# Kernel optimization log

Hardware: AMD Instinct MI355X
Metric: run time of the kernel (lower is better)

Reference implementation:

```python
import jax, jax.numpy as jnp
import numpy as np

TOP_K = 2
LB_WEIGHT = 0.01
Z_WEIGHT = 0.001


def setup_inputs() -> dict:
    key = jax.random.key(0)
    ks = jax.random.split(key, 5)
    B, S, D, F, E = 4, 2048, 1024, 2048, 8
    x = jax.random.normal(ks[0], (B, S, D), dtype=jnp.float32)
    Wr = jax.random.normal(ks[1], (D, E), dtype=jnp.float32) / np.sqrt(D).astype(np.float32)
    Wg = jax.random.normal(ks[2], (E, D, F), dtype=jnp.float32) / np.sqrt(D).astype(np.float32)
    Wu = jax.random.normal(ks[3], (E, D, F), dtype=jnp.float32) / np.sqrt(D).astype(np.float32)
    Wd = jax.random.normal(ks[4], (E, F, D), dtype=jnp.float32) / np.sqrt(F).astype(np.float32)
    return {"x": x, "Wr": Wr, "Wg": Wg, "Wu": Wu, "Wd": Wd}


def reference(x, Wr, Wg, Wu, Wd):
    B, S, D = x.shape
    E = Wr.shape[1]
    xf = x.reshape(-1, D)                       # [T, D]
    T = xf.shape[0]

    logits = xf @ Wr                            # [T, E]
    probs = jax.nn.softmax(logits, axis=-1)
    topv, topi = jax.lax.top_k(probs, TOP_K)    # [T, K]
    topv = topv / jnp.sum(topv, axis=-1, keepdims=True)

    # combine[t, e] = renormalized top-k prob if expert e selected for token t, else 0
    onehot = jax.nn.one_hot(topi, E, dtype=x.dtype)          # [T, K, E]
    combine = jnp.sum(onehot * topv[..., None], axis=1)      # [T, E]

    out = jnp.zeros_like(xf)
    for e in range(E):  # fixed small expert count; dense compute masked by combine weights
        h = jax.nn.silu(xf @ Wg[e]) * (xf @ Wu[e])           # [T, F] SwiGLU
        out = out + combine[:, e:e + 1] * (h @ Wd[e])

    # auxiliary losses
    counts = jnp.sum(onehot, axis=(0, 1))                    # [E] tokens routed per expert
    f_i = counts / (T * TOP_K)
    P_i = jnp.mean(probs, axis=0)
    load_balance = E * jnp.sum(f_i * P_i)
    z_loss = jnp.mean(jax.nn.logsumexp(logits, axis=-1) ** 2)
    aux_loss = LB_WEIGHT * load_balance + Z_WEIGHT * z_loss

    return out.reshape(B, S, D), aux_loss
```

## Files before the change

### kernel.cpp

```cpp
#include <hip/hip_runtime.h>
#include <cstdint>

#define T_TOK 8192
#define Dm 1024
#define Fm 2048
#define Em 8

typedef unsigned short u16;
typedef __attribute__((ext_vector_type(8))) short short8;
typedef __attribute__((ext_vector_type(4))) float floatx4;

__device__ __forceinline__ u16 f2bf(float f) {
  union { float f; unsigned u; } v; v.f = f;
  unsigned r = v.u + 0x7fffu + ((v.u >> 16) & 1u);
  return (u16)(r >> 16);
}

__device__ __forceinline__ void gld_lds16(const void* g, void* l) {
  __builtin_amdgcn_global_load_lds(
      (const __attribute__((address_space(1))) void*)g,
      (__attribute__((address_space(3))) void*)l, 16, 0, 0);
}

__global__ void zero_meta(int* counts, int* offc, float* psum, float* zsum) {
  int t = threadIdx.x;
  if (t < 8) { counts[t] = 0; offc[t] = 0; psum[t] = 0.f; }
  if (t == 8) zsum[0] = 0.f;
}

__global__ __launch_bounds__(256) void prep_kernel(
    const float* __restrict__ Wg, const float* __restrict__ Wu, const float* __restrict__ Wd,
    u16* __restrict__ WgT, u16* __restrict__ WuT, u16* __restrict__ WdT,
    const float* __restrict__ x, const float* __restrict__ Wr, u16* __restrict__ xb,
    int* __restrict__ topi, float* __restrict__ topw,
    int* __restrict__ counts, float* __restrict__ psum, float* __restrict__ zsum) {
  __shared__ __align__(16) char smem[33056];
  int tid = threadIdx.x;
  if (blockIdx.x >= 256) {
    u16* tile = (u16*)smem;
    int bid = blockIdx.x - 256;
    int m = bid >> 9, t = bid & 511;
    int type = m >> 3, e = m & 7;
    const float* src; u16* dst; int R, C, csh;
    if (type == 0)      { src = Wg; dst = WgT; R = Dm; C = Fm; csh = 5; }
    else if (type == 1) { src = Wu; dst = WuT; R = Dm; C = Fm; csh = 5; }
    else                { src = Wd; dst = WdT; R = Fm; C = Dm; csh = 4; }
    int ty = t >> csh, tx = t & ((1 << csh) - 1);
    int r0 = ty * 64, c0 = tx * 64;
    const float* s = src + (size_t)e * R * C;
    u16* d = dst + (size_t)e * C * R;
#pragma unroll
    for (int p = 0; p < 16; ++p) {
      int idx = p * 256 + tid;
      int i = idx >> 6, j = idx & 63;
      tile[i * 66 + j] = f2bf(s[(size_t)(r0 + i) * C + (c0 + j)]);
    }
    __syncthreads();
#pragma unroll
    for (int p = 0; p < 16; ++p) {
      int idx = p * 256 + tid;
      int i = idx >> 6, j = idx & 63;
      d[(size_t)(c0 + i) * R + (r0 + j)] = tile[j * 66 + i];
    }
    return;
  }
  int rb = blockIdx.x;
  float* wr_s = (float*)smem;
  float (*redf)[9] = (float(*)[9])(smem + 32768);
  int (*redi)[8] = (int(*)[8])(smem + 32768 + 144);
  for (int i = tid; i < Dm * Em; i += 256) wr_s[i] = Wr[i];
  __syncthreads();
  int wv = tid >> 6, lane = tid & 63;
  float pl[8] = {0, 0, 0, 0, 0, 0, 0, 0};
  float zl = 0.f;
  int cl[8] = {0, 0, 0, 0, 0, 0, 0, 0};
  for (int it = 0; it < 8; ++it) {
    int t = (rb * 4 + wv) * 8 + it;
    const float* xt = x + (size_t)t * Dm;
    u16* xbt = xb + (size_t)t * Dm;
    float acc[8] = {0, 0, 0, 0, 0, 0, 0, 0};
#pragma unroll
    for (int i = 0; i < 16; ++i) {
      int dd = i * 64 + lane;
      float xv = xt[dd];
      xbt[dd] = f2bf(xv);
#pragma unroll
      for (int e2 = 0; e2 < 8; ++e2) acc[e2] += xv * wr_s[dd * 8 + e2];
    }
#pragma unroll
    for (int e2 = 0; e2 < 8; ++e2) {
      float v = acc[e2];
      for (int o = 32; o > 0; o >>= 1) v += __shfl_down(v, o);
      acc[e2] = v;
    }
    if (lane == 0) {
      float m = acc[0];
#pragma unroll
      for (int e2 = 1; e2 < 8; ++e2) m = fmaxf(m, acc[e2]);
      float p[8]; float s = 0.f;
#pragma unroll
      for (int e2 = 0; e2 < 8; ++e2) { p[e2] = expf(acc[e2] - m); s += p[e2]; }
      float inv = 1.f / s;
#pragma unroll
      for (int e2 = 0; e2 < 8; ++e2) { p[e2] *= inv; pl[e2] += p[e2]; }
      float lse = m + logf(s);
      zl += lse * lse;
      int i1 = 0;
#pragma unroll
      for (int e2 = 1; e2 < 8; ++e2) if (p[e2] > p[i1]) i1 = e2;
      int i2 = -1; float b2 = -1e30f;
#pragma unroll
      for (int e2 = 0; e2 < 8; ++e2)
        if (e2 != i1 && p[e2] > b2) { b2 = p[e2]; i2 = e2; }
      float ssum = p[i1] + p[i2];
      topi[2 * t] = i1; topi[2 * t + 1] = i2;
      topw[2 * t] = p[i1] / ssum; topw[2 * t + 1] = p[i2] / ssum;
      cl[i1]++; cl[i2]++;
    }
  }
  if (lane == 0) {
#pragma unroll
    for (int e2 = 0; e2 < 8; ++e2) { redf[wv][e2] = pl[e2]; redi[wv][e2] = cl[e2]; }
    redf[wv][8] = zl;
  }
  __syncthreads();
  if (tid < 8) {
    atomicAdd(&psum[tid], redf[0][tid] + redf[1][tid] + redf[2][tid] + redf[3][tid]);
    atomicAdd(&counts[tid], redi[0][tid] + redi[1][tid] + redi[2][tid] + redi[3][tid]);
  } else if (tid == 8) {
    atomicAdd(zsum, redf[0][8] + redf[1][8] + redf[2][8] + redf[3][8]);
  }
}

__global__ __launch_bounds__(256) void scatter_kernel(
    const int* __restrict__ topi, const float* __restrict__ topw,
    const int* __restrict__ counts, const float* __restrict__ psum, const float* __restrict__ zsum,
    int* __restrict__ offc, int* __restrict__ etok, float* __restrict__ ew,
    int* __restrict__ slots, int* __restrict__ bases, float* __restrict__ out_aux) {
  __shared__ int lcnt[8];
  __shared__ int lbase[8];
  __shared__ int basesS[8];
  int tid = threadIdx.x;
  if (blockIdx.x == 0 && tid == 0) {
    float lb = 0.f;
    for (int e = 0; e < 8; ++e)
      lb += ((float)counts[e] / (2.f * T_TOK)) * (psum[e] / (float)T_TOK);
    lb *= 8.f;
    float z = zsum[0] / (float)T_TOK;
    *out_aux = 0.01f * lb + 0.001f * z;
  }
  if (tid < 8) {
    lcnt[tid] = 0;
    int b = 0;
    for (int e = 0; e < tid; ++e) b += counts[e];
    basesS[tid] = b;
    if (blockIdx.x == 0) bases[tid] = b;
  }
  __syncthreads();
  int t = blockIdx.x * 256 + tid;
  int e0 = topi[2 * t], e1 = topi[2 * t + 1];
  int lp0 = atomicAdd(&lcnt[e0], 1);
  int lp1 = atomicAdd(&lcnt[e1], 1);
  __syncthreads();
  if (tid < 8) lbase[tid] = atomicAdd(&offc[tid], lcnt[tid]);
  __syncthreads();
  int p0 = basesS[e0] + lbase[e0] + lp0;
  etok[p0] = t; ew[p0] = topw[2 * t]; slots[2 * t] = p0;
  int p1 = basesS[e1] + lbase[e1] + lp1;
  etok[p1] = t; ew[p1] = topw[2 * t + 1]; slots[2 * t + 1] = p1;
}

__global__ __launch_bounds__(256, 3) void gemm1_kernel(
    const u16* __restrict__ xb, const u16* __restrict__ WgT, const u16* __restrict__ WuT,
    u16* __restrict__ h, const int* __restrict__ etok,
    const int* __restrict__ counts, const int* __restrict__ bases) {
  const int e = blockIdx.z;
  const int Ne = counts[e];
  const int m0 = blockIdx.y * 128;
  if (m0 >= Ne) return;
  const int n0 = blockIdx.x * 64;
  const int be = bases[e];

  __shared__ __align__(16) u16 As[128 * 64];
  __shared__ __align__(16) u16 Bgs[64 * 64];
  __shared__ __align__(16) u16 Bus[64 * 64];

  const int tid = threadIdx.x;
  const int wv = tid >> 6, lane = tid & 63;
  const int wr = wv >> 1, wc = wv & 1;
  const int srow = tid >> 3;
  const int cg = (tid & 7) ^ (srow & 7);
  const u16* wg_e = WgT + (size_t)e * Fm * Dm;
  const u16* wu_e = WuT + (size_t)e * Fm * Dm;

  const u16* ag[4]; const u16* bgp[2]; const u16* bup[2];
#pragma unroll
  for (int j = 0; j < 4; ++j) {
    int row = 32 * j + srow;
    int rr = m0 + row; rr = rr < Ne ? rr : Ne - 1;
    int tok = etok[be + rr];
    ag[j] = xb + (size_t)tok * Dm + cg * 8;
  }
#pragma unroll
  for (int j = 0; j < 2; ++j) {
    int row = 32 * j + srow;
    bgp[j] = wg_e + (size_t)(n0 + row) * Dm + cg * 8;
    bup[j] = wu_e + (size_t)(n0 + row) * Dm + cg * 8;
  }
  const int lbase = 8 * wv * 64 + lane * 8;

  floatx4 accg[4][2], accu[4][2];
#pragma unroll
  for (int mi = 0; mi < 4; ++mi)
#pragma unroll
    for (int ni = 0; ni < 2; ++ni) { accg[mi][ni] = (floatx4)0.f; accu[mi][ni] = (floatx4)0.f; }

  for (int k0 = 0; k0 < Dm; k0 += 64) {
    __syncthreads();
#pragma unroll
    for (int j = 0; j < 4; ++j) gld_lds16(ag[j] + k0, &As[lbase + 32 * j * 64]);
#pragma unroll
    for (int j = 0; j < 2; ++j) {
      int lo = lbase + 32 * j * 64;
      gld_lds16(bgp[j] + k0, &Bgs[lo]);
      gld_lds16(bup[j] + k0, &Bus[lo]);
    }
    __syncthreads();
#pragma unroll
    for (int ks = 0; ks < 2; ++ks) {
      short8 af[4], bgf[2], buf_[2];
      const int col = lane & 15, quad = lane >> 4;
      const int c = ks * 4 + quad;
#pragma unroll
      for (int mi = 0; mi < 4; ++mi) {
        int row = wr * 64 + mi * 16 + col;
        af[mi] = *(const short8*)&As[row * 64 + ((c ^ (row & 7)) << 3)];
      }
#pragma unroll
      for (int ni = 0; ni < 2; ++ni) {
        int row = wc * 32 + ni * 16 + col;
        int o = row * 64 + ((c ^ (row & 7)) << 3);
        bgf[ni] = *(const short8*)&Bgs[o];
        buf_[ni] = *(const short8*)&Bus[o];
      }
#pragma unroll
      for (int mi = 0; mi < 4; ++mi)
#pragma unroll
        for (int ni = 0; ni < 2; ++ni) {
          accg[mi][ni] = __builtin_amdgcn_mfma_f32_16x16x32_bf16(af[mi], bgf[ni], accg[mi][ni], 0, 0, 0);
          accu[mi][ni] = __builtin_amdgcn_mfma_f32_16x16x32_bf16(af[mi], buf_[ni], accu[mi][ni], 0, 0, 0);
        }
    }
  }
  const int col = lane & 15, quad = lane >> 4;
#pragma unroll
  for (int mi = 0; mi < 4; ++mi)
#pragma unroll
    for (int ni = 0; ni < 2; ++ni) {
      int f = n0 + wc * 32 + ni * 16 + col;
#pragma unroll
      for (int r = 0; r < 4; ++r) {
        int lrow = wr * 64 + mi * 16 + quad * 4 + r;
        if (m0 + lrow < Ne) {
          float gv = accg[mi][ni][r];
          float hv = (gv / (1.f + expf(-gv))) * accu[mi][ni][r];
          h[(size_t)(be + m0 + lrow) * Fm + f] = f2bf(hv);
        }
      }
    }
}

__global__ __launch_bounds__(256, 3) void gemm2_kernel(
    const u16* __restrict__ h, const u16* __restrict__ WdT, float* __restrict__ h2,
    const float* __restrict__ ew,
    const int* __restrict__ counts, const int* __restrict__ bases) {
  const int e = blockIdx.z;
  const int Ne = counts[e];
  const int m0 = blockIdx.y * 128;
  if (m0 >= Ne) return;
  const int n0 = blockIdx.x * 64;
  const int be = bases[e];

  __shared__ __align__(16) u16 As[128 * 64];
  __shared__ __align__(16) u16 Bs[64 * 64];
  __shared__ float wS[128];

  const int tid = threadIdx.x;
  if (tid < 128) {
    int rr = m0 + tid; rr = rr < Ne ? rr : Ne - 1;
    wS[tid] = ew[be + rr];
  }
  const int wv = tid >> 6, lane = tid & 63;
  const int wr = wv >> 1, wc = wv & 1;
  const int srow = tid >> 3;
  const int cg = (tid & 7) ^ (srow & 7);
  const u16* wd_e = WdT + (size_t)e * Dm * Fm;

  const u16* ap[4]; const u16* bp[2];
#pragma unroll
  for (int j = 0; j < 4; ++j) {
    int row = 32 * j + srow;
    int rr = m0 + row; rr = rr < Ne ? rr : Ne - 1;
    ap[j] = h + (size_t)(be + rr) * Fm + cg * 8;
  }
#pragma unroll
  for (int j = 0; j < 2; ++j) {
    int row = 32 * j + srow;
    bp[j] = wd_e + (size_t)(n0 + row) * Fm + cg * 8;
  }
  const int lbase = 8 * wv * 64 + lane * 8;

  floatx4 acc[4][2];
#pragma unroll
  for (int mi = 0; mi < 4; ++mi)
#pragma unroll
    for (int ni = 0; ni < 2; ++ni) acc[mi][ni] = (floatx4)0.f;

  for (int k0 = 0; k0 < Fm; k0 += 64) {
    __syncthreads();
#pragma unroll
    for (int j = 0; j < 4; ++j) gld_lds16(ap[j] + k0, &As[lbase + 32 * j * 64]);
#pragma unroll
    for (int j = 0; j < 2; ++j) gld_lds16(bp[j] + k0, &Bs[lbase + 32 * j * 64]);
    __syncthreads();
#pragma unroll
    for (int ks = 0; ks < 2; ++ks) {
      short8 af[4], bf[2];
      const int col = lane & 15, quad = lane >> 4;
      const int c = ks * 4 + quad;
#pragma unroll
      for (int mi = 0; mi < 4; ++mi) {
        int row = wr * 64 + mi * 16 + col;
        af[mi] = *(const short8*)&As[row * 64 + ((c ^ (row & 7)) << 3)];
      }
#pragma unroll
      for (int ni = 0; ni < 2; ++ni) {
        int row = wc * 32 + ni * 16 + col;
        bf[ni] = *(const short8*)&Bs[row * 64 + ((c ^ (row & 7)) << 3)];
      }
#pragma unroll
      for (int mi = 0; mi < 4; ++mi)
#pragma unroll
        for (int ni = 0; ni < 2; ++ni)
          acc[mi][ni] = __builtin_amdgcn_mfma_f32_16x16x32_bf16(af[mi], bf[ni], acc[mi][ni], 0, 0, 0);
    }
  }
  const int col = lane & 15, quad = lane >> 4;
#pragma unroll
  for (int mi = 0; mi < 4; ++mi)
#pragma unroll
    for (int ni = 0; ni < 2; ++ni) {
      int oc = n0 + wc * 32 + ni * 16 + col;
#pragma unroll
      for (int r = 0; r < 4; ++r) {
        int lrow = wr * 64 + mi * 16 + quad * 4 + r;
        if (m0 + lrow < Ne)
          h2[(size_t)(be + m0 + lrow) * Dm + oc] = acc[mi][ni][r] * wS[lrow];
      }
    }
}

__global__ __launch_bounds__(256) void combine_kernel(
    const float* __restrict__ h2, const int* __restrict__ slots, float* __restrict__ out) {
  int t = blockIdx.x;
  int d4 = threadIdx.x;
  int s0 = slots[2 * t], s1 = slots[2 * t + 1];
  const float4* r0 = (const float4*)(h2 + (size_t)s0 * Dm);
  const float4* r1 = (const float4*)(h2 + (size_t)s1 * Dm);
  float4 a = r0[d4], b = r1[d4];
  float4 o = make_float4(a.x + b.x, a.y + b.y, a.z + b.z, a.w + b.w);
  ((float4*)(out + (size_t)t * Dm))[d4] = o;
}

extern "C" void kernel_launch(void* const* d_in, const int* in_sizes, int n_in,
                              void* d_out, int out_size, void* d_ws, size_t ws_size,
                              hipStream_t stream) {
  const float* x = (const float*)d_in[0];
  const float* Wr = (const float*)d_in[1];
  const float* Wg = (const float*)d_in[2];
  const float* Wu = (const float*)d_in[3];
  const float* Wd = (const float*)d_in[4];
  float* out = (float*)d_out;

  char* p = (char*)d_ws;
  auto take = [&](size_t bytes) { char* r = p; p += (bytes + 255) & ~(size_t)255; return r; };
  u16* WgT = (u16*)take((size_t)Em * Fm * Dm * 2);
  u16* WuT = (u16*)take((size_t)Em * Fm * Dm * 2);
  u16* WdT = (u16*)take((size_t)Em * Dm * Fm * 2);
  u16* xb = (u16*)take((size_t)T_TOK * Dm * 2);
  u16* gh = (u16*)take((size_t)2 * T_TOK * Fm * 2);
  int* topi = (int*)take((size_t)T_TOK * 2 * 4);
  float* topw = (float*)take((size_t)T_TOK * 2 * 4);
  int* etok = (int*)take((size_t)2 * T_TOK * 4);
  float* ew = (float*)take((size_t)2 * T_TOK * 4);
  int* slots = (int*)take((size_t)2 * T_TOK * 4);
  int* counts = (int*)take(64);
  int* bases = (int*)take(64);
  int* offc = (int*)take(64);
  float* psum = (float*)take(64);
  float* zsum = (float*)take(64);
  float* h2 = (float*)WgT;

  zero_meta<<<1, 64, 0, stream>>>(counts, offc, psum, zsum);
  prep_kernel<<<dim3(24 * 512 + 256), 256, 0, stream>>>(
      Wg, Wu, Wd, WgT, WuT, WdT, x, Wr, xb, topi, topw, counts, psum, zsum);
  scatter_kernel<<<dim3(T_TOK / 256), 256, 0, stream>>>(
      topi, topw, counts, psum, zsum, offc, etok, ew, slots, bases, out + (size_t)T_TOK * Dm);
  gemm1_kernel<<<dim3(Fm / 64, 64, Em), 256, 0, stream>>>(xb, WgT, WuT, gh, etok, counts, bases);
  gemm2_kernel<<<dim3(Dm / 64, 64, Em), 256, 0, stream>>>(gh, WdT, h2, ew, counts, bases);
  combine_kernel<<<dim3(T_TOK), 256, 0, stream>>>(h2, slots, out);
}
```

Baseline: 523.5 us.

## Enlarge MoE GEMM tiles and add 4-stage async LDS pipeline with priority hints

Both expert GEMMs move to 512-thread blocks with larger output tiles (256x128 for gate/up, 256x256 for down) and a K-step of 32 staged through a 4-deep ring of LDS buffers. Global-to-LDS loads are issued three stages ahead, and each step has one barrier gated by explicit vmcnt waits. MFMA bursts are wrapped in s_setprio so that memory traffic overlaps compute and fewer barriers are paid per unit of work. In exchange, register and LDS use per block rise (128KB LDS), partially filled M tiles waste more work, and the grids have fewer blocks.

```diff
diff --git a/kernel.cpp b/kernel.cpp
--- a/kernel.cpp
+++ b/kernel.cpp
@@ -170,97 +170,122 @@
   etok[p1] = t; ew[p1] = topw[2 * t + 1]; slots[2 * t + 1] = p1;
 }
 
-__global__ __launch_bounds__(256, 3) void gemm1_kernel(
+__global__ __launch_bounds__(512, 2) void gemm1_kernel(
     const u16* __restrict__ xb, const u16* __restrict__ WgT, const u16* __restrict__ WuT,
     u16* __restrict__ h, const int* __restrict__ etok,
     const int* __restrict__ counts, const int* __restrict__ bases) {
   const int e = blockIdx.z;
   const int Ne = counts[e];
-  const int m0 = blockIdx.y * 128;
+  const int m0 = blockIdx.y * 256;
   if (m0 >= Ne) return;
-  const int n0 = blockIdx.x * 64;
+  const int n0 = blockIdx.x * 128;
   const int be = bases[e];
 
-  __shared__ __align__(16) u16 As[128 * 64];
-  __shared__ __align__(16) u16 Bgs[64 * 64];
-  __shared__ __align__(16) u16 Bus[64 * 64];
+  __shared__ __align__(16) u16 lds[4 * 16384];
 
   const int tid = threadIdx.x;
-  const int wv = tid >> 6, lane = tid & 63;
-  const int wr = wv >> 1, wc = wv & 1;
-  const int srow = tid >> 3;
-  const int cg = (tid & 7) ^ (srow & 7);
+  const int lane = tid & 63, wv = tid >> 6;
+  const int wm = wv >> 2, wn = wv & 3;
+  const int col = lane & 15, quad = lane >> 4;
+
+  const int srow = tid >> 2;
+  const int cg = (tid & 3) ^ ((srow >> 2) & 3);
+  const int ldst = tid * 8;
+
   const u16* wg_e = WgT + (size_t)e * Fm * Dm;
   const u16* wu_e = WuT + (size_t)e * Fm * Dm;
 
-  const u16* ag[4]; const u16* bgp[2]; const u16* bup[2];
-#pragma unroll
-  for (int j = 0; j < 4; ++j) {
-    int row = 32 * j + srow;
-    int rr = m0 + row; rr = rr < Ne ? rr : Ne - 1;
-    int tok = etok[be + rr];
-    ag[j] = xb + (size_t)tok * Dm + cg * 8;
-  }
+  const u16* ag[2];
 #pragma unroll
   for (int j = 0; j < 2; ++j) {
-    int row = 32 * j + srow;
-    bgp[j] = wg_e + (size_t)(n0 + row) * Dm + cg * 8;
-    bup[j] = wu_e + (size_t)(n0 + row) * Dm + cg * 8;
-  }
-  const int lbase = 8 * wv * 64 + lane * 8;
-
-  floatx4 accg[4][2], accu[4][2];
-#pragma unroll
-  for (int mi = 0; mi < 4; ++mi)
+    int row = m0 + j * 128 + srow;
+    int rr = row < Ne ? row : Ne - 1;
+    ag[j] = xb + (size_t)etok[be + rr] * Dm + cg * 8;
+  }
+  const u16* bgp = wg_e + (size_t)(n0 + srow) * Dm + cg * 8;
+  const u16* bup = wu_e + (size_t)(n0 + srow) * Dm + cg * 8;
+
+  floatx4 accg[8][2], accu[8][2];
+#pragma unroll
+  for (int mi = 0; mi < 8; ++mi)
 #pragma unroll
     for (int ni = 0; ni < 2; ++ni) { accg[mi][ni] = (floatx4)0.f; accu[mi][ni] = (floatx4)0.f; }
 
-  for (int k0 = 0; k0 < Dm; k0 += 64) {
-    __syncthreads();
-#pragma unroll
-    for (int j = 0; j < 4; ++j) gld_lds16(ag[j] + k0, &As[lbase + 32 * j * 64]);
-#pragma unroll
-    for (int j = 0; j < 2; ++j) {
-      int lo = lbase + 32 * j * 64;
-      gld_lds16(bgp[j] + k0, &Bgs[lo]);
-      gld_lds16(bup[j] + k0, &Bus[lo]);
-    }
-    __syncthreads();
-#pragma unroll
-    for (int ks = 0; ks < 2; ++ks) {
-      short8 af[4], bgf[2], buf_[2];
-      const int col = lane & 15, quad = lane >> 4;
-      const int c = ks * 4 + quad;
-#pragma unroll
-      for (int mi = 0; mi < 4; ++mi) {
-        int row = wr * 64 + mi * 16 + col;
-        af[mi] = *(const short8*)&As[row * 64 + ((c ^ (row & 7)) << 3)];
+#define G1_STAGE_A(t) { u16* b_ = &lds[((t) & 3) * 16384]; int k0_ = (t) * 32; \
+    gld_lds16(ag[0] + k0_, b_ + ldst); gld_lds16(ag[1] + k0_, b_ + 4096 + ldst); }
+#define G1_STAGE_B(t) { u16* b_ = &lds[((t) & 3) * 16384]; int k0_ = (t) * 32; \
+    gld_lds16(bgp + k0_, b_ + 8192 + ldst); gld_lds16(bup + k0_, b_ + 12288 + ldst); }
+
+  G1_STAGE_A(0); G1_STAGE_B(0);
+  G1_STAGE_A(1); G1_STAGE_B(1);
+  G1_STAGE_A(2); G1_STAGE_B(2);
+  asm volatile("s_waitcnt vmcnt(8)" ::: "memory");
+  __builtin_amdgcn_s_barrier();
+  asm volatile("" ::: "memory");
+  __builtin_amdgcn_sched_barrier(0);
+
+  for (int t = 0; t < 32; ++t) {
+    const u16* Ab = &lds[(t & 3) * 16384];
+    const u16* Gb = Ab + 8192;
+    const u16* Ub = Ab + 12288;
+    short8 bgf[2], buf_[2], af[4];
+#pragma unroll
+    for (int ni = 0; ni < 2; ++ni) {
+      int row = wn * 32 + ni * 16 + col;
+      int o = row * 32 + (((quad ^ (row >> 2)) & 3) << 3);
+      bgf[ni] = *(const short8*)&Gb[o];
+      buf_[ni] = *(const short8*)&Ub[o];
+    }
+#pragma unroll
+    for (int mi = 0; mi < 4; ++mi) {
+      int row = wm * 128 + mi * 16 + col;
+      af[mi] = *(const short8*)&Ab[row * 32 + (((quad ^ (row >> 2)) & 3) << 3)];
+    }
+    if (t + 3 < 32) G1_STAGE_A(t + 3);
+    __builtin_amdgcn_s_setprio(1);
+#pragma unroll
+    for (int mi = 0; mi < 4; ++mi)
+#pragma unroll
+      for (int ni = 0; ni < 2; ++ni) {
+        accg[mi][ni] = __builtin_amdgcn_mfma_f32_16x16x32_bf16(af[mi], bgf[ni], accg[mi][ni], 0, 0, 0);
+        accu[mi][ni] = __builtin_amdgcn_mfma_f32_16x16x32_bf16(af[mi], buf_[ni], accu[mi][ni], 0, 0, 0);
       }
+    __builtin_amdgcn_s_setprio(0);
+#pragma unroll
+    for (int mi = 0; mi < 4; ++mi) {
+      int row = wm * 128 + (mi + 4) * 16 + col;
+      af[mi] = *(const short8*)&Ab[row * 32 + (((quad ^ (row >> 2)) & 3) << 3)];
+    }
+    if (t + 3 < 32) G1_STAGE_B(t + 3);
+    __builtin_amdgcn_s_setprio(1);
+#pragma unroll
+    for (int mi = 0; mi < 4; ++mi)
 #pragma unroll
       for (int ni = 0; ni < 2; ++ni) {
-        int row = wc * 32 + ni * 16 + col;
-        int o = row * 64 + ((c ^ (row & 7)) << 3);
-        bgf[ni] = *(const short8*)&Bgs[o];
-        buf_[ni] = *(const short8*)&Bus[o];
+        accg[mi + 4][ni] = __builtin_amdgcn_mfma_f32_16x16x32_bf16(af[mi], bgf[ni], accg[mi + 4][ni], 0, 0, 0);
+        accu[mi + 4][ni] = __builtin_amdgcn_mfma_f32_16x16x32_bf16(af[mi], buf_[ni], accu[mi + 4][ni], 0, 0, 0);
       }
-#pragma unroll
-      for (int mi = 0; mi < 4; ++mi)
-#pragma unroll
-        for (int ni = 0; ni < 2; ++ni) {
-          accg[mi][ni] = __builtin_amdgcn_mfma_f32_16x16x32_bf16(af[mi], bgf[ni], accg[mi][ni], 0, 0, 0);
-          accu[mi][ni] = __builtin_amdgcn_mfma_f32_16x16x32_bf16(af[mi], buf_[ni], accu[mi][ni], 0, 0, 0);
-        }
-    }
-  }
-  const int col = lane & 15, quad = lane >> 4;
-#pragma unroll
-  for (int mi = 0; mi < 4; ++mi)
+    __builtin_amdgcn_s_setprio(0);
+    if (t + 3 < 32)      { asm volatile("s_waitcnt vmcnt(8)" ::: "memory"); }
+    else if (t + 2 < 32) { asm volatile("s_waitcnt vmcnt(4)" ::: "memory"); }
+    else if (t + 1 < 32) { asm volatile("s_waitcnt vmcnt(0)" ::: "memory"); }
+    if (t + 1 < 32) {
+      __builtin_amdgcn_s_barrier();
+      asm volatile("" ::: "memory");
+      __builtin_amdgcn_sched_barrier(0);
+    }
+  }
+#undef G1_STAGE_A
+#undef G1_STAGE_B
+
+#pragma unroll
+  for (int mi = 0; mi < 8; ++mi)
 #pragma unroll
     for (int ni = 0; ni < 2; ++ni) {
-      int f = n0 + wc * 32 + ni * 16 + col;
+      int f = n0 + wn * 32 + ni * 16 + col;
 #pragma unroll
       for (int r = 0; r < 4; ++r) {
-        int lrow = wr * 64 + mi * 16 + quad * 4 + r;
+        int lrow = wm * 128 + mi * 16 + quad * 4 + r;
         if (m0 + lrow < Ne) {
           float gv = accg[mi][ni][r];
           float hv = (gv / (1.f + expf(-gv))) * accu[mi][ni][r];
@@ -270,90 +295,118 @@
     }
 }
 
-__global__ __launch_bounds__(256, 3) void gemm2_kernel(
+__global__ __launch_bounds__(512, 2) void gemm2_kernel(
     const u16* __restrict__ h, const u16* __restrict__ WdT, float* __restrict__ h2,
     const float* __restrict__ ew,
     const int* __restrict__ counts, const int* __restrict__ bases) {
   const int e = blockIdx.z;
   const int Ne = counts[e];
-  const int m0 = blockIdx.y * 128;
+  const int m0 = blockIdx.y * 256;
   if (m0 >= Ne) return;
-  const int n0 = blockIdx.x * 64;
+  const int n0 = blockIdx.x * 256;
   const int be = bases[e];
 
-  __shared__ __align__(16) u16 As[128 * 64];
-  __shared__ __align__(16) u16 Bs[64 * 64];
-  __shared__ float wS[128];
+  __shared__ __align__(16) u16 lds[4 * 16384];
+  __shared__ float wS[256];
 
   const int tid = threadIdx.x;
-  if (tid < 128) {
+  if (tid < 256) {
     int rr = m0 + tid; rr = rr < Ne ? rr : Ne - 1;
     wS[tid] = ew[be + rr];
   }
-  const int wv = tid >> 6, lane = tid & 63;
-  const int wr = wv >> 1, wc = wv & 1;
-  const int srow = tid >> 3;
-  const int cg = (tid & 7) ^ (srow & 7);
+  const int lane = tid & 63, wv = tid >> 6;
+  const int wm = wv >> 2, wn = wv & 3;
+  const int col = lane & 15, quad = lane >> 4;
+
+  const int srow = tid >> 2;
+  const int cg = (tid & 3) ^ ((srow >> 2) & 3);
+  const int ldst = tid * 8;
+
   const u16* wd_e = WdT + (size_t)e * Dm * Fm;
 
-  const u16* ap[4]; const u16* bp[2];
-#pragma unroll
-  for (int j = 0; j < 4; ++j) {
-    int row = 32 * j + srow;
-    int rr = m0 + row; rr = rr < Ne ? rr : Ne - 1;
+  const u16* ap[2]; const u16* bp[2];
+#pragma unroll
+  for (int j = 0; j < 2; ++j) {
+    int row = m0 + j * 128 + srow;
+    int rr = row < Ne ? row : Ne - 1;
     ap[j] = h + (size_t)(be + rr) * Fm + cg * 8;
-  }
-#pragma unroll
-  for (int j = 0; j < 2; ++j) {
-    int row = 32 * j + srow;
-    bp[j] = wd_e + (size_t)(n0 + row) * Fm + cg * 8;
-  }
-  const int lbase = 8 * wv * 64 + lane * 8;
-
-  floatx4 acc[4][2];
-#pragma unroll
-  for (int mi = 0; mi < 4; ++mi)
-#pragma unroll
-    for (int ni = 0; ni < 2; ++ni) acc[mi][ni] = (floatx4)0.f;
-
-  for (int k0 = 0; k0 < Fm; k0 += 64) {
-    __syncthreads();
-#pragma unroll
-    for (int j = 0; j < 4; ++j) gld_lds16(ap[j] + k0, &As[lbase + 32 * j * 64]);
-#pragma unroll
-    for (int j = 0; j < 2; ++j) gld_lds16(bp[j] + k0, &Bs[lbase + 32 * j * 64]);
-    __syncthreads();
-#pragma unroll
-    for (int ks = 0; ks < 2; ++ks) {
-      short8 af[4], bf[2];
-      const int col = lane & 15, quad = lane >> 4;
-      const int c = ks * 4 + quad;
-#pragma unroll
-      for (int mi = 0; mi < 4; ++mi) {
-        int row = wr * 64 + mi * 16 + col;
-        af[mi] = *(const short8*)&As[row * 64 + ((c ^ (row & 7)) << 3)];
-      }
-#pragma unroll
-      for (int ni = 0; ni < 2; ++ni) {
-        int row = wc * 32 + ni * 16 + col;
-        bf[ni] = *(const short8*)&Bs[row * 64 + ((c ^ (row & 7)) << 3)];
-      }
-#pragma unroll
-      for (int mi = 0; mi < 4; ++mi)
-#pragma unroll
-        for (int ni = 0; ni < 2; ++ni)
-          acc[mi][ni] = __builtin_amdgcn_mfma_f32_16x16x32_bf16(af[mi], bf[ni], acc[mi][ni], 0, 0, 0);
-    }
-  }
-  const int col = lane & 15, quad = lane >> 4;
-#pragma unroll
-  for (int mi = 0; mi < 4; ++mi)
-#pragma unroll
-    for (int ni = 0; ni < 2; ++ni) {
-      int oc = n0 + wc * 32 + ni * 16 + col;
+    bp[j] = wd_e + (size_t)(n0 + j * 128 + srow) * Fm + cg * 8;
+  }
+
+  floatx4 acc[8][4];
+#pragma unroll
+  for (int mi = 0; mi < 8; ++mi)
+#pragma unroll
+    for (int ni = 0; ni < 4; ++ni) acc[mi][ni] = (floatx4)0.f;
+
+#define G2_STAGE_A(t) { u16* b_ = &lds[((t) & 3) * 16384]; int k0_ = (t) * 32; \
+    gld_lds16(ap[0] + k0_, b_ + ldst); gld_lds16(ap[1] + k0_, b_ + 4096 + ldst); }
+#define G2_STAGE_B(t) { u16* b_ = &lds[((t) & 3) * 16384]; int k0_ = (t) * 32; \
+    gld_lds16(bp[0] + k0_, b_ + 8192 + ldst); gld_lds16(bp[1] + k0_, b_ + 12288 + ldst); }
+
+  G2_STAGE_A(0); G2_STAGE_B(0);
+  G2_STAGE_A(1); G2_STAGE_B(1);
+  G2_STAGE_A(2); G2_STAGE_B(2);
+  asm volatile("s_waitcnt vmcnt(8)" ::: "memory");
+  __builtin_amdgcn_s_barrier();
+  asm volatile("" ::: "memory");
+  __builtin_amdgcn_sched_barrier(0);
+
+  for (int t = 0; t < 64; ++t) {
+    const u16* Ab = &lds[(t & 3) * 16384];
+    const u16* Bb = Ab + 8192;
+    short8 bf[4], af[4];
+#pragma unroll
+    for (int ni = 0; ni < 4; ++ni) {
+      int row = wn * 64 + ni * 16 + col;
+      bf[ni] = *(const short8*)&Bb[row * 32 + (((quad ^ (row >> 2)) & 3) << 3)];
+    }
+#pragma unroll
+    for (int mi = 0; mi < 4; ++mi) {
+      int row = wm * 128 + mi * 16 + col;
+      af[mi] = *(const short8*)&Ab[row * 32 + (((quad ^ (row >> 2)) & 3) << 3)];
+    }
+    if (t + 3 < 64) G2_STAGE_A(t + 3);
+    __builtin_amdgcn_s_setprio(1);
+#pragma unroll
+    for (int mi = 0; mi < 4; ++mi)
+#pragma unroll
+      for (int ni = 0; ni < 4; ++ni)
+        acc[mi][ni] = __builtin_amdgcn_mfma_f32_16x16x32_bf16(af[mi], bf[ni], acc[mi][ni], 0, 0, 0);
+    __builtin_amdgcn_s_setprio(0);
+#pragma unroll
+    for (int mi = 0; mi < 4; ++mi) {
+      int row = wm * 128 + (mi + 4) * 16 + col;
+      af[mi] = *(const short8*)&Ab[row * 32 + (((quad ^ (row >> 2)) & 3) << 3)];
+    }
+    if (t + 3 < 64) G2_STAGE_B(t + 3);
+    __builtin_amdgcn_s_setprio(1);
+#pragma unroll
+    for (int mi = 0; mi < 4; ++mi)
+#pragma unroll
+      for (int ni = 0; ni < 4; ++ni)
+        acc[mi + 4][ni] = __builtin_amdgcn_mfma_f32_16x16x32_bf16(af[mi], bf[ni], acc[mi + 4][ni], 0, 0, 0);
+    __builtin_amdgcn_s_setprio(0);
+    if (t + 3 < 64)      { asm volatile("s_waitcnt vmcnt(8)" ::: "memory"); }
+    else if (t + 2 < 64) { asm volatile("s_waitcnt vmcnt(4)" ::: "memory"); }
+    else if (t + 1 < 64) { asm volatile("s_waitcnt vmcnt(0)" ::: "memory"); }
+    if (t + 1 < 64) {
+      __builtin_amdgcn_s_barrier();
+      asm volatile("" ::: "memory");
+      __builtin_amdgcn_sched_barrier(0);
+    }
+  }
+#undef G2_STAGE_A
+#undef G2_STAGE_B
+
+#pragma unroll
+  for (int mi = 0; mi < 8; ++mi)
+#pragma unroll
+    for (int ni = 0; ni < 4; ++ni) {
+      int oc = n0 + wn * 64 + ni * 16 + col;
 #pragma unroll
       for (int r = 0; r < 4; ++r) {
-        int lrow = wr * 64 + mi * 16 + quad * 4 + r;
+        int lrow = wm * 128 + mi * 16 + quad * 4 + r;
         if (m0 + lrow < Ne)
           h2[(size_t)(be + m0 + lrow) * Dm + oc] = acc[mi][ni][r] * wS[lrow];
       }
@@ -406,7 +459,7 @@
       Wg, Wu, Wd, WgT, WuT, WdT, x, Wr, xb, topi, topw, counts, psum, zsum);
   scatter_kernel<<<dim3(T_TOK / 256), 256, 0, stream>>>(
       topi, topw, counts, psum, zsum, offc, etok, ew, slots, bases, out + (size_t)T_TOK * Dm);
-  gemm1_kernel<<<dim3(Fm / 64, 64, Em), 256, 0, stream>>>(xb, WgT, WuT, gh, etok, counts, bases);
-  gemm2_kernel<<<dim3(Dm / 64, 64, Em), 256, 0, stream>>>(gh, WdT, h2, ew, counts, bases);
+  gemm1_kernel<<<dim3(Fm / 128, 32, Em), 512, 0, stream>>>(xb, WgT, WuT, gh, etok, counts, bases);
+  gemm2_kernel<<<dim3(Dm / 256, 32, Em), 512, 0, stream>>>(gh, WdT, h2, ew, counts, bases);
   combine_kernel<<<dim3(T_TOK), 256, 0, stream>>>(h2, slots, out);
 }
```

After: 549.6 us. +5.0%, slower.

## Switch expert GEMMs to 32x32x16 MFMA and widen gemm2 N-tile

Applied to the files above, without the earlier changes.

Both expert GEMM kernels now use the 32x32x16 bf16 MFMA with 16-float accumulators in place of the 16x16x32 variant. This cuts the number of LDS fragment loads per MFMA and the instruction count. gemm2 also doubles its output tile width to 128 columns, which halves the grid in x and improves reuse of the A tile loaded from h. The larger tile raises LDS use and may reduce occupancy, and the epilogue store pattern now writes strided rows per register.

```diff
diff --git a/kernel.cpp b/kernel.cpp
--- a/kernel.cpp
+++ b/kernel.cpp
@@ -8,7 +8,7 @@
 
 typedef unsigned short u16;
 typedef __attribute__((ext_vector_type(8))) short short8;
-typedef __attribute__((ext_vector_type(4))) float floatx4;
+typedef __attribute__((ext_vector_type(16))) float floatx16;
 
 __device__ __forceinline__ u16 f2bf(float f) {
   union { float f; unsigned u; } v; v.f = f;
@@ -209,11 +209,13 @@
   }
   const int lbase = 8 * wv * 64 + lane * 8;
 
-  floatx4 accg[4][2], accu[4][2];
-#pragma unroll
-  for (int mi = 0; mi < 4; ++mi)
-#pragma unroll
-    for (int ni = 0; ni < 2; ++ni) { accg[mi][ni] = (floatx4)0.f; accu[mi][ni] = (floatx4)0.f; }
+  floatx16 accg[2], accu[2];
+#pragma unroll
+  for (int mt = 0; mt < 2; ++mt) { accg[mt] = (floatx16)0.f; accu[mt] = (floatx16)0.f; }
+
+  const int r32 = lane & 31, half = lane >> 5;
+  const int rowa0 = wr * 64 + r32;
+  const int rn = wc * 32 + r32;
 
   for (int k0 = 0; k0 < Dm; k0 += 64) {
     __syncthreads();
@@ -227,45 +229,29 @@
     }
     __syncthreads();
 #pragma unroll
-    for (int ks = 0; ks < 2; ++ks) {
-      short8 af[4], bgf[2], buf_[2];
-      const int col = lane & 15, quad = lane >> 4;
-      const int c = ks * 4 + quad;
-#pragma unroll
-      for (int mi = 0; mi < 4; ++mi) {
-        int row = wr * 64 + mi * 16 + col;
-        af[mi] = *(const short8*)&As[row * 64 + ((c ^ (row & 7)) << 3)];
-      }
-#pragma unroll
-      for (int ni = 0; ni < 2; ++ni) {
-        int row = wc * 32 + ni * 16 + col;
-        int o = row * 64 + ((c ^ (row & 7)) << 3);
-        bgf[ni] = *(const short8*)&Bgs[o];
-        buf_[ni] = *(const short8*)&Bus[o];
-      }
-#pragma unroll
-      for (int mi = 0; mi < 4; ++mi)
-#pragma unroll
-        for (int ni = 0; ni < 2; ++ni) {
-          accg[mi][ni] = __builtin_amdgcn_mfma_f32_16x16x32_bf16(af[mi], bgf[ni], accg[mi][ni], 0, 0, 0);
-          accu[mi][ni] = __builtin_amdgcn_mfma_f32_16x16x32_bf16(af[mi], buf_[ni], accu[mi][ni], 0, 0, 0);
-        }
-    }
-  }
-  const int col = lane & 15, quad = lane >> 4;
-#pragma unroll
-  for (int mi = 0; mi < 4; ++mi)
-#pragma unroll
-    for (int ni = 0; ni < 2; ++ni) {
-      int f = n0 + wc * 32 + ni * 16 + col;
-#pragma unroll
-      for (int r = 0; r < 4; ++r) {
-        int lrow = wr * 64 + mi * 16 + quad * 4 + r;
-        if (m0 + lrow < Ne) {
-          float gv = accg[mi][ni][r];
-          float hv = (gv / (1.f + expf(-gv))) * accu[mi][ni][r];
-          h[(size_t)(be + m0 + lrow) * Fm + f] = f2bf(hv);
-        }
+    for (int ks = 0; ks < 4; ++ks) {
+      const int c = ks * 2 + half;
+      short8 af0 = *(const short8*)&As[rowa0 * 64 + ((c ^ (rowa0 & 7)) << 3)];
+      short8 af1 = *(const short8*)&As[(rowa0 + 32) * 64 + ((c ^ (rowa0 & 7)) << 3)];
+      int ob = rn * 64 + ((c ^ (rn & 7)) << 3);
+      short8 bg = *(const short8*)&Bgs[ob];
+      short8 bu = *(const short8*)&Bus[ob];
+      accg[0] = __builtin_amdgcn_mfma_f32_32x32x16_bf16(af0, bg, accg[0], 0, 0, 0);
+      accu[0] = __builtin_amdgcn_mfma_f32_32x32x16_bf16(af0, bu, accu[0], 0, 0, 0);
+      accg[1] = __builtin_amdgcn_mfma_f32_32x32x16_bf16(af1, bg, accg[1], 0, 0, 0);
+      accu[1] = __builtin_amdgcn_mfma_f32_32x32x16_bf16(af1, bu, accu[1], 0, 0, 0);
+    }
+  }
+  const int f = n0 + wc * 32 + r32;
+#pragma unroll
+  for (int mt = 0; mt < 2; ++mt)
+#pragma unroll
+    for (int reg = 0; reg < 16; ++reg) {
+      int lrow = wr * 64 + mt * 32 + (reg & 3) + 8 * (reg >> 2) + 4 * half;
+      if (m0 + lrow < Ne) {
+        float gv = accg[mt][reg];
+        float hv = (gv / (1.f + expf(-gv))) * accu[mt][reg];
+        h[(size_t)(be + m0 + lrow) * Fm + f] = f2bf(hv);
       }
     }
 }
@@ -278,11 +264,11 @@
   const int Ne = counts[e];
   const int m0 = blockIdx.y * 128;
   if (m0 >= Ne) return;
-  const int n0 = blockIdx.x * 64;
+  const int n0 = blockIdx.x * 128;
   const int be = bases[e];
 
   __shared__ __align__(16) u16 As[128 * 64];
-  __shared__ __align__(16) u16 Bs[64 * 64];
+  __shared__ __align__(16) u16 Bs[128 * 64];
   __shared__ float wS[128];
 
   const int tid = threadIdx.x;
@@ -296,68 +282,59 @@
   const int cg = (tid & 7) ^ (srow & 7);
   const u16* wd_e = WdT + (size_t)e * Dm * Fm;
 
-  const u16* ap[4]; const u16* bp[2];
+  const u16* ap[4]; const u16* bp[4];
 #pragma unroll
   for (int j = 0; j < 4; ++j) {
     int row = 32 * j + srow;
     int rr = m0 + row; rr = rr < Ne ? rr : Ne - 1;
     ap[j] = h + (size_t)(be + rr) * Fm + cg * 8;
-  }
-#pragma unroll
-  for (int j = 0; j < 2; ++j) {
-    int row = 32 * j + srow;
     bp[j] = wd_e + (size_t)(n0 + row) * Fm + cg * 8;
   }
   const int lbase = 8 * wv * 64 + lane * 8;
 
-  floatx4 acc[4][2];
-#pragma unroll
-  for (int mi = 0; mi < 4; ++mi)
-#pragma unroll
-    for (int ni = 0; ni < 2; ++ni) acc[mi][ni] = (floatx4)0.f;
+  floatx16 acc[2][2];
+#pragma unroll
+  for (int mt = 0; mt < 2; ++mt)
+#pragma unroll
+    for (int nt = 0; nt < 2; ++nt) acc[mt][nt] = (floatx16)0.f;
+
+  const int r32 = lane & 31, half = lane >> 5;
+  const int rowa0 = wr * 64 + r32;
+  const int rowb0 = wc * 64 + r32;
 
   for (int k0 = 0; k0 < Fm; k0 += 64) {
     __syncthreads();
 #pragma unroll
     for (int j = 0; j < 4; ++j) gld_lds16(ap[j] + k0, &As[lbase + 32 * j * 64]);
 #pragma unroll
-    for (int j = 0; j < 2; ++j) gld_lds16(bp[j] + k0, &Bs[lbase + 32 * j * 64]);
-    __syncthreads();
-#pragma unroll
-    for (int ks = 0; ks < 2; ++ks) {
-      short8 af[4], bf[2];
-      const int col = lane & 15, quad = lane >> 4;
-      const int c = ks * 4 + quad;
-#pragma unroll
-      for (int mi = 0; mi < 4; ++mi) {
-        int row = wr * 64 + mi * 16 + col;
-        af[mi] = *(const short8*)&As[row * 64 + ((c ^ (row & 7)) << 3)];
+    for (int j = 0; j < 4; ++j) gld_lds16(bp[j] + k0, &Bs[lbase + 32 * j * 64]);
+    __syncthreads();
+#pragma unroll
+    for (int ks = 0; ks < 4; ++ks) {
+      const int c = ks * 2 + half;
+      int oa = (c ^ (rowa0 & 7)) << 3;
+      int obo = (c ^ (rowb0 & 7)) << 3;
+      short8 af0 = *(const short8*)&As[rowa0 * 64 + oa];
+      short8 af1 = *(const short8*)&As[(rowa0 + 32) * 64 + oa];
+      short8 bf0 = *(const short8*)&Bs[rowb0 * 64 + obo];
+      short8 bf1 = *(const short8*)&Bs[(rowb0 + 32) * 64 + obo];
+      acc[0][0] = __builtin_amdgcn_mfma_f32_32x32x16_bf16(af0, bf0, acc[0][0], 0, 0, 0);
+      acc[0][1] = __builtin_amdgcn_mfma_f32_32x32x16_bf16(af0, bf1, acc[0][1], 0, 0, 0);
+      acc[1][0] = __builtin_amdgcn_mfma_f32_32x32x16_bf16(af1, bf0, acc[1][0], 0, 0, 0);
+      acc[1][1] = __builtin_amdgcn_mfma_f32_32x32x16_bf16(af1, bf1, acc[1][1], 0, 0, 0);
+    }
+  }
+  const int ocb = n0 + wc * 64 + r32;
+#pragma unroll
+  for (int mt = 0; mt < 2; ++mt)
+#pragma unroll
+    for (int nt = 0; nt < 2; ++nt)
+#pragma unroll
+      for (int reg = 0; reg < 16; ++reg) {
+        int lrow = wr * 64 + mt * 32 + (reg & 3) + 8 * (reg >> 2) + 4 * half;
+        if (m0 + lrow < Ne)
+          h2[(size_t)(be + m0 + lrow) * Dm + ocb + nt * 32] = acc[mt][nt][reg] * wS[lrow];
       }
-#pragma unroll
-      for (int ni = 0; ni < 2; ++ni) {
-        int row = wc * 32 + ni * 16 + col;
-        bf[ni] = *(const short8*)&Bs[row * 64 + ((c ^ (row & 7)) << 3)];
-      }
-#pragma unroll
-      for (int mi = 0; mi < 4; ++mi)
-#pragma unroll
-        for (int ni = 0; ni < 2; ++ni)
-          acc[mi][ni] = __builtin_amdgcn_mfma_f32_16x16x32_bf16(af[mi], bf[ni], acc[mi][ni], 0, 0, 0);
-    }
-  }
-  const int col = lane & 15, quad = lane >> 4;
-#pragma unroll
-  for (int mi = 0; mi < 4; ++mi)
-#pragma unroll
-    for (int ni = 0; ni < 2; ++ni) {
-      int oc = n0 + wc * 32 + ni * 16 + col;
-#pragma unroll
-      for (int r = 0; r < 4; ++r) {
-        int lrow = wr * 64 + mi * 16 + quad * 4 + r;
-        if (m0 + lrow < Ne)
-          h2[(size_t)(be + m0 + lrow) * Dm + oc] = acc[mi][ni][r] * wS[lrow];
-      }
-    }
 }
 
 __global__ __launch_bounds__(256) void combine_kernel(
@@ -407,6 +384,6 @@
   scatter_kernel<<<dim3(T_TOK / 256), 256, 0, stream>>>(
       topi, topw, counts, psum, zsum, offc, etok, ew, slots, bases, out + (size_t)T_TOK * Dm);
   gemm1_kernel<<<dim3(Fm / 64, 64, Em), 256, 0, stream>>>(xb, WgT, WuT, gh, etok, counts, bases);
-  gemm2_kernel<<<dim3(Dm / 64, 64, Em), 256, 0, stream>>>(gh, WdT, h2, ew, counts, bases);
+  gemm2_kernel<<<dim3(Dm / 128, 64, Em), 256, 0, stream>>>(gh, WdT, h2, ew, counts, bases);
   combine_kernel<<<dim3(T_TOK), 256, 0, stream>>>(h2, slots, out);
 }
```

New measurement: 536.0 us. 1.02x slower.
